# Kernel tuning notes

Measured on AMD Instinct MI355X. Metric: run time of the kernel, lower is better.

Reference implementation:

```python
import jax, jax.numpy as jnp
import numpy as np

V, D, DC, L, K, H, ND, S, B = 16, 256, 128, 3, 16, 4, 3, 900, 16
HD = D // H
DMETA = 17           # [confidence(1) | layer_id(8) | iter(4) | pass(4)]
DSLOT = DC + DMETA
MAX_ITERS, MAX_PASSES, WRITE_TOK = 2, 2, 64
FLOATS = ['token_embed','segment_embed','slot_embeddings','layer_id_embeddings',
          'Wq_read','Wk_read','Wv_read','Wg_read','bg_read','Wqkv','Wo',
          'Wwk','Wwv','Wwg','bwg','Wout','bout','prev_answer_embed','Wfb','bfb']


def setup_inputs():
    key = jax.random.key(0)
    ks = jax.random.split(key, 24)
    n = lambda i, shape: 0.02 * jax.random.normal(ks[i], shape, dtype=jnp.float32)
    return dict(
        demo_inputs=jax.random.randint(ks[0], (B, ND, S), 0, V),
        demo_outputs=jax.random.randint(ks[1], (B, ND, S), 0, V),
        test_input=jax.random.randint(ks[2], (B, S), 0, V),
        token_embed=n(3, (V, D)), segment_embed=n(4, (2, D)),
        slot_embeddings=n(5, (L, K, DC)), layer_id_embeddings=n(6, (L, 8)),
        Wq_read=n(7, (L, D, DC)), Wk_read=n(8, (L, DSLOT, DC)), Wv_read=n(9, (L, DSLOT, D)),
        Wg_read=n(10, (L, D, 1)), bg_read=jnp.zeros((L, 1)),
        Wqkv=n(11, (L, D, 3 * D)), Wo=n(12, (L, D, D)),
        Wwk=n(13, (L, D, DC)), Wwv=n(14, (L, D, DC)),
        Wwg=n(15, (L, 2 * DC, 1)), bwg=jnp.zeros((L, 1)),
        Wout=n(16, (D, V)), bout=jnp.zeros((V,)),
        prev_answer_embed=n(17, (V, D)),
        Wfb=n(18, (2 * D, D)), bfb=jnp.zeros((D,)),
    )


def make_rope(n, hd):
    inv = 1.0 / (10000.0 ** (jnp.arange(0, hd, 2, dtype=jnp.float32) / hd))
    f = jnp.arange(n, dtype=jnp.float32)[:, None] * inv[None, :]  # [N, hd/2]
    return jnp.cos(f), jnp.sin(f)


def apply_rope(x, cos, sin):  # x: [B,H,N,hd]
    x1, x2 = x[..., ::2], x[..., 1::2]
    r1 = x1 * cos - x2 * sin
    r2 = x1 * sin + x2 * cos
    return jnp.stack([r1, r2], axis=-1).reshape(x.shape)


def layer_step(h, cache, l, it, pas, cos, sin, p):
    Bsz, N, _ = h.shape
    s0 = l * K
    # --- read: cross-attention from sequence to full structured cache ---
    q = h @ p['Wq_read'][l]                                   # [B,N,DC]
    k = cache @ p['Wk_read'][l]                               # [B,LK,DC]
    v = cache @ p['Wv_read'][l]                               # [B,LK,D]
    attn = jax.nn.softmax(jnp.einsum('bnd,bmd->bnm', q, k) / np.float32(np.sqrt(DC)), axis=-1)
    read = jnp.einsum('bnm,bmd->bnd', attn, v)
    rgate = jax.nn.sigmoid(h @ p['Wg_read'][l] + p['bg_read'][l])
    h = h + rgate * read
    # --- linear self-attention with RoPE (use_linear_attention=True) ---
    qh, kh, vh = jnp.split(h @ p['Wqkv'][l], 3, axis=-1)
    heads = lambda x: x.reshape(Bsz, N, H, HD).transpose(0, 2, 1, 3)
    qh, kh, vh = heads(qh), heads(kh), heads(vh)
    qf = jax.nn.elu(apply_rope(qh, cos, sin)) + 1.0
    kf = jax.nn.elu(apply_rope(kh, cos, sin)) + 1.0
    kv = jnp.einsum('bhnd,bhne->bhde', kf, vh)                # [B,H,HD,HD]
    z = 1.0 / (jnp.einsum('bhnd,bhd->bhn', qf, kf.sum(axis=2)) + 1e-6)
    att = jnp.einsum('bhnd,bhde->bhne', qf, kv) * z[..., None]
    h = h + att.transpose(0, 2, 1, 3).reshape(Bsz, N, D) @ p['Wo'][l]
    # --- write: last max_write_tokens tokens -> this layer's slot block ---
    wt = h[:, -WRITE_TOK:]                                    # [B,64,D]
    wk, wv = wt @ p['Wwk'][l], wt @ p['Wwv'][l]               # [B,64,DC]
    sq = cache[:, s0:s0 + K, :DC]                             # slot content queries
    wattn = jax.nn.softmax(jnp.einsum('bkd,bmd->bkm', sq, wk) / np.float32(np.sqrt(DC)), axis=-1)
    new_c = jnp.einsum('bkm,bmd->bkd', wattn, wv)
    wgate = jax.nn.sigmoid(jnp.concatenate([sq, new_c], -1) @ p['Wwg'][l] + p['bwg'][l])
    it_oh = jax.nn.one_hot(min(it, 3), 4, dtype=h.dtype)
    ps_oh = jax.nn.one_hot(min(pas, 3), 4, dtype=h.dtype)
    cache = cache.at[:, s0:s0 + K, :DC].set(sq + wgate * new_c)
    cache = cache.at[:, s0:s0 + K, DC:DC + 1].set(wgate)      # confidence
    cache = cache.at[:, s0:s0 + K, DC + 9:DC + 13].set(jnp.broadcast_to(it_oh, (Bsz, K, 4)))
    cache = cache.at[:, s0:s0 + K, DC + 13:].set(jnp.broadcast_to(ps_oh, (Bsz, K, 4)))
    return h, cache


def _model(p, demo_inputs, demo_outputs, test_input):
    Bsz = test_input.shape[0]
    # interleave demo_in/demo_out pairs then append test input
    demos = jnp.stack([demo_inputs, demo_outputs], axis=2).reshape(Bsz, ND * 2 * S)
    full = jnp.concatenate([demos, test_input], axis=1)       # [B, 6300]
    N = full.shape[1]
    cur = p['token_embed'][full] + p['segment_embed'][0]      # [B,N,D]
    cos, sin = make_rope(N, HD)
    # initial cache: learned content | conf=0 | layer_id | iter=0 | pass=0
    content = jnp.broadcast_to(p['slot_embeddings'].reshape(L * K, DC), (Bsz, L * K, DC))
    lids = jnp.broadcast_to(p['layer_id_embeddings'][:, None, :], (L, K, 8)).reshape(L * K, 8)
    meta = jnp.concatenate([jnp.zeros((L * K, 1)), lids, jnp.zeros((L * K, 8))], axis=-1)
    cache = jnp.concatenate([content, jnp.broadcast_to(meta, (Bsz, L * K, DMETA))], axis=-1)
    ts = ND * 2 * S
    prev_logits = None
    for pas in range(MAX_PASSES):
        if pas > 0:  # answer feedback from previous pass predictions
            pae = p['prev_answer_embed'][jnp.argmax(prev_logits, axis=-1)]
            tr = cur[:, ts:ts + S]
            g = jax.nn.sigmoid(jnp.concatenate([tr, pae], -1) @ p['Wfb'] + p['bfb'])
            cur = cur.at[:, ts:ts + S].set(tr + g * pae)
        h = cur
        for l in range(L):
            for it in range(MAX_ITERS):
                h, cache = layer_step(h, cache, l, it, pas, cos, sin, p)
        prev_logits = h[:, ts:ts + S] @ p['Wout'] + p['bout']  # [B,S,V]
    return prev_logits


def reference(demo_inputs, demo_outputs, test_input, token_embed, segment_embed,
              slot_embeddings, layer_id_embeddings, Wq_read, Wk_read, Wv_read,
              Wg_read, bg_read, Wqkv, Wo, Wwk, Wwv, Wwg, bwg, Wout, bout,
              prev_answer_embed, Wfb, bfb):
    p = dict(zip(FLOATS, (token_embed, segment_embed, slot_embeddings, layer_id_embeddings,
                          Wq_read, Wk_read, Wv_read, Wg_read, bg_read, Wqkv, Wo,
                          Wwk, Wwv, Wwg, bwg, Wout, bout, prev_answer_embed, Wfb, bfb)))
    return _model(p, demo_inputs, demo_outputs, test_input)
```

## Files before the change

### kernel.cpp

```cpp
#include <hip/hip_runtime.h>
#include <math.h>

#define Bz 16
#define Sz 900
#define Vz 16
#define Dz 256
#define DCz 128
#define Hz 4
#define Nz 6300
#define TSz 5400
#define DSLOTz 145
#define NSLOTz 48
#define GXA 99

typedef unsigned short u16;
typedef unsigned int u32;

typedef __bf16 bf16x8 __attribute__((ext_vector_type(8)));
typedef float floatx4 __attribute__((ext_vector_type(4)));
union U8 { bf16x8 v; uint4 q; };

static __device__ __forceinline__ float sigm(float x){ return 1.0f/(1.0f+__expf(-x)); }
static __device__ __forceinline__ void fma4(float4& a, float s, float4 b){ a.x+=s*b.x; a.y+=s*b.y; a.z+=s*b.z; a.w+=s*b.w; }
static __device__ __forceinline__ float dot4(float4 a, float4 b){ return a.x*b.x + a.y*b.y + a.z*b.z + a.w*b.w; }
static __device__ __forceinline__ float4 f4z(){ float4 z; z.x=0.f; z.y=0.f; z.z=0.f; z.w=0.f; return z; }
static __device__ __forceinline__ float elu1(float x){ return x>0.f ? x+1.f : __expf(x); }
static __device__ __forceinline__ float fcomp(float4 v, int i){ return (i==0)?v.x:(i==1)?v.y:(i==2)?v.z:v.w; }

static __device__ __forceinline__ uint hi16(float x){
  uint u = __float_as_uint(x);
  return (u + 0x7fffu + ((u>>16)&1u)) >> 16;
}

typedef const void GV __attribute__((address_space(1)));
typedef void LV __attribute__((address_space(3)));
static __device__ __forceinline__ void gl16(const float* g, float* l){
  __builtin_amdgcn_global_load_lds((GV*)g, (LV*)l, 16, 0, 0);
}
static __device__ __forceinline__ void gl16b(const void* g, void* l){
  __builtin_amdgcn_global_load_lds((GV*)g, (LV*)l, 16, 0, 0);
}

__global__ void k_sentinel(float* out, int nelem){
  int i = blockIdx.x*256 + threadIdx.x;
  if (i < nelem) out[i] = 12345.0f;
}

__global__ void k_zero(float* p, int n){
  int i = blockIdx.x*256 + threadIdx.x;
  if (i < n) p[i] = 0.f;
}

__global__ void k_rope(float* cost, float* sint){
  int i = blockIdx.x*256 + threadIdx.x;
  if (i >= Nz*32) return;
  int n = i>>5, f = i&31;
  double invd = pow(10000.0, -(double)f/32.0);
  double fr = (double)n * invd;
  cost[i] = (float)cos(fr);
  sint[i] = (float)sin(fr);
}

__global__ void k_embed(const int* __restrict__ di, const int* __restrict__ dq,
                        const int* __restrict__ ti, const float* __restrict__ temb,
                        const float* __restrict__ semb, float* __restrict__ h){
  int i = blockIdx.x*256 + threadIdx.x;
  if (i >= Bz*Nz*64) return;
  int dv = i & 63; int bn = i >> 6; int n = bn % Nz; int b = bn / Nz;
  int tok;
  if (n < TSz){
    int nd = n/1800; int r = n - nd*1800;
    tok = (r < Sz) ? di[(b*3+nd)*Sz + r] : dq[(b*3+nd)*Sz + (r-Sz)];
  } else {
    tok = ti[b*Sz + (n-TSz)];
  }
  const float4* e4 = (const float4*)(temb + (size_t)tok*Dz);
  const float4* s4 = (const float4*)semb;
  float4 v = e4[dv]; float4 s = s4[dv];
  v.x += s.x; v.y += s.y; v.z += s.z; v.w += s.w;
  ((float4*)h)[(size_t)bn*64 + dv] = v;
}

__global__ void k_cache_init(const float* __restrict__ slot_emb, const float* __restrict__ lid,
                             float* __restrict__ cache){
  int i = blockIdx.x*256 + threadIdx.x;
  if (i >= Bz*NSLOTz*DSLOTz) return;
  int c = i % DSLOTz; int sc = (i / DSLOTz) % NSLOTz; int l = sc >> 4;
  float v = 0.f;
  if (c < DCz) v = slot_emb[sc*DCz + c];
  else if (c >= 129 && c < 137) v = lid[l*8 + (c-129)];
  cache[i] = v;
}

__global__ void k_pack_w(const float* __restrict__ Wqkv,
                         u16* __restrict__ wh, u16* __restrict__ wl){
  int i = blockIdx.x*256 + threadIdx.x;
  if (i >= 3*65536) return;
  int l = i >> 16; int r = i & 65535;
  int ks = r >> 13; int ct = (r>>9)&15; int lane = (r>>3)&63; int e = r&7;
  int k = ks*32 + ((lane>>4)<<3) + e;
  int c = ct*16 + (lane&15);
  float x = Wqkv[(size_t)l*196608 + (size_t)k*768 + c];
  uint hb = hi16(x);
  uint lb = hi16(x - __uint_as_float(hb<<16));
  wh[i] = (u16)hb; wl[i] = (u16)lb;
}

__global__ void k_pack_wkv(const float* __restrict__ Wqkv,
                           u16* __restrict__ wh, u16* __restrict__ wl){
  int i = blockIdx.x*256 + threadIdx.x;
  if (i >= 3*131072) return;
  int l = i / 131072; int r = i % 131072;
  int ks = r >> 14; int ct = (r>>9)&31; int lane = (r>>3)&63; int e = r&7;
  int k = ks*32 + ((lane>>4)<<3) + e;
  int c = ct*16 + (lane&15);
  float x = Wqkv[(size_t)l*196608 + (size_t)k*768 + 256 + c];
  uint hb = hi16(x);
  uint lb = hi16(x - __uint_as_float(hb<<16));
  wh[i] = (u16)hb; wl[i] = (u16)lb;
}

__global__ void k_pack_wr(const float* __restrict__ Wqr,
                          u16* __restrict__ wh, u16* __restrict__ wl){
  int i = blockIdx.x*256 + threadIdx.x;
  if (i >= 3*32768) return;
  int l = i >> 15; int r = i & 32767;
  int ks = r >> 12; int ct = (r>>9)&7; int lane = (r>>3)&63; int e = r&7;
  int k = ks*32 + ((lane>>4)<<3) + e;
  int c = ct*16 + (lane&15);
  float x = Wqr[(size_t)l*32768 + (size_t)k*DCz + c];
  uint hb = hi16(x);
  uint lb = hi16(x - __uint_as_float(hb<<16));
  wh[i] = (u16)hb; wl[i] = (u16)lb;
}

__global__ void k_pack_p(const float* __restrict__ pmat,
                         u16* __restrict__ ph, u16* __restrict__ pl){
  int i = blockIdx.x*256 + threadIdx.x;
  if (i >= 16*65536) return;
  int b = i >> 16; int r = i & 65535;
  int ks2 = r >> 13; int ct = (r>>9)&15; int lane = (r>>3)&63; int e = r&7;
  int c = ks2*32 + ((lane>>4)<<3) + e;
  int oc = ct*16 + (lane&15);
  float x = pmat[(((size_t)(b*4 + (c>>6)))*64 + (c&63))*256 + oc];
  uint hb = hi16(x);
  uint lb = hi16(x - __uint_as_float(hb<<16));
  ph[i] = (u16)hb; pl[i] = (u16)lb;
}

__global__ __launch_bounds__(384) void k_proj_cache(const float* __restrict__ cache,
    const float* __restrict__ Wk, const float* __restrict__ Wv,
    u16* __restrict__ krh, u16* __restrict__ krl,
    u16* __restrict__ vrh, u16* __restrict__ vrl){
  __shared__ float crow[DSLOTz];
  int b = blockIdx.x / NSLOTz, sc = blockIdx.x % NSLOTz;
  int t = threadIdx.x;
  const float* cp = cache + (size_t)(b*NSLOTz+sc)*DSLOTz;
  if (t < DSLOTz) crow[t] = cp[t];
  __syncthreads();
  if (t < DCz){
    float a = 0.f;
    for (int r2=0;r2<DSLOTz;r2++) a += crow[r2]*Wk[r2*DCz + t];
    uint hb = hi16(a);
    uint lb = hi16(a - __uint_as_float(hb<<16));
    int ks = t>>5, st = sc>>4, lane = (sc&15) | (((t>>3)&3)<<4), e = t&7;
    size_t idx = (size_t)b*6144 + (size_t)(((ks*3+st)*64 + lane)*8 + e);
    krh[idx] = (u16)hb; krl[idx] = (u16)lb;
  } else {
    int d = t - DCz;
    float a = 0.f;
    for (int r2=0;r2<DSLOTz;r2++) a += crow[r2]*Wv[r2*Dz + d];
    uint hb = hi16(a);
    uint lb = hi16(a - __uint_as_float(hb<<16));
    int ot = d>>4, ks2 = sc>>5, lane = (d&15) | (((sc>>3)&3)<<4), e = sc&7;
    size_t idx = (size_t)b*16384 + (size_t)(((ks2*16+ot)*64 + lane)*8 + e);
    vrh[idx] = (u16)hb; vrl[idx] = (u16)lb;
  }
}

#define RA2_BH 0
#define RA2_BL 5120
#define RA2_QBH 10240
#define RA2_QBL 30720
#define RA2_ABH 10240
#define RA2_ABL 20480
#define RA2_G  51200
#define RA2_WG 51456
__global__ __launch_bounds__(256) void k_read_attn(
    float* __restrict__ h,
    const u16* __restrict__ wqh, const u16* __restrict__ wql,
    const u16* __restrict__ krh, const u16* __restrict__ krl,
    const u16* __restrict__ vrh, const u16* __restrict__ vrl,
    const float* __restrict__ Wg, const float* __restrict__ bg){
  __shared__ float smem[13120];
  char* sb = (char*)smem;
  const int t = threadIdx.x;
  const int b = blockIdx.y;
  const int n0 = blockIdx.x*64;
  const int w = t>>6, lane = t&63, ln = t&15, lq = (t>>4)&3;
  float* hb = h + (size_t)b*Nz*Dz;
  ((float*)(sb+RA2_WG))[t] = Wg[t];
  floatx4 acc[2][4];
  #pragma unroll
  for (int i=0;i<2;i++)
    #pragma unroll
    for (int j=0;j<4;j++){ acc[i][j][0]=0.f; acc[i][j][1]=0.f; acc[i][j][2]=0.f; acc[i][j][3]=0.f; }
  for (int ks=0; ks<8; ks++){
    __syncthreads();
    {
      int n = n0 + (t>>2);
      const float* hp = hb + (size_t)n*Dz + ks*32 + (t&3)*8;
      float x[8];
      if (n < Nz){
        float4 v0 = *(const float4*)(hp);
        float4 v1 = *(const float4*)(hp+4);
        x[0]=v0.x; x[1]=v0.y; x[2]=v0.z; x[3]=v0.w;
        x[4]=v1.x; x[5]=v1.y; x[6]=v1.z; x[7]=v1.w;
      } else {
        #pragma unroll
        for (int e=0;e<8;e++) x[e]=0.f;
      }
      uint hw[4], lw[4];
      #pragma unroll
      for (int e=0;e<4;e++){
        uint h0=hi16(x[2*e]), h1=hi16(x[2*e+1]);
        uint l0=hi16(x[2*e]-__uint_as_float(h0<<16));
        uint l1=hi16(x[2*e+1]-__uint_as_float(h1<<16));
        hw[e]=h0|(h1<<16); lw[e]=l0|(l1<<16);
      }
      int a16 = (((t>>2)*5 + (t&3))<<4);
      *(uint4*)(sb + RA2_BH + a16) = make_uint4(hw[0],hw[1],hw[2],hw[3]);
      *(uint4*)(sb + RA2_BL + a16) = make_uint4(lw[0],lw[1],lw[2],lw[3]);
    }
    __syncthreads();
    U8 bh[4], bl[4];
    #pragma unroll
    for (int nt=0; nt<4; nt++){
      int a16 = (((nt*16+ln)*5 + lq)<<4);
      bh[nt].q = *(const uint4*)(sb + RA2_BH + a16);
      bl[nt].q = *(const uint4*)(sb + RA2_BL + a16);
    }
    #pragma unroll
    for (int mf=0; mf<2; mf++){
      U8 ah, al;
      size_t ai = ((size_t)(ks*8 + w*2 + mf))*512 + lane*8;
      ah.q = *(const uint4*)(wqh + ai);
      al.q = *(const uint4*)(wql + ai);
      #pragma unroll
      for (int nt=0; nt<4; nt++){
        acc[mf][nt] = __builtin_amdgcn_mfma_f32_16x16x32_bf16(ah.v, bh[nt].v, acc[mf][nt], 0,0,0);
        acc[mf][nt] = __builtin_amdgcn_mfma_f32_16x16x32_bf16(ah.v, bl[nt].v, acc[mf][nt], 0,0,0);
        acc[mf][nt] = __builtin_amdgcn_mfma_f32_16x16x32_bf16(al.v, bh[nt].v, acc[mf][nt], 0,0,0);
      }
    }
  }
  {
    int n = t>>2, kq = t&3;
    int nn = n0+n; int nc = (nn < Nz) ? nn : (Nz-1);
    const float* hp = hb + (size_t)nc*Dz + kq*64;
    const float* wgp = (const float*)(sb+RA2_WG) + kq*64;
    float a = 0.f;
    for (int k=0;k<64;k+=4){
      float4 hv = *(const float4*)(hp+k);
      float4 wv = *(const float4*)(wgp+k);
      a += dot4(hv,wv);
    }
    a += __shfl_xor(a,1,64);
    a += __shfl_xor(a,2,64);
    if (kq==0) ((float*)(sb+RA2_G))[n] = a;
  }
  {
    #pragma unroll
    for (int mf=0; mf<2; mf++){
      #pragma unroll
      for (int nt=0; nt<4; nt++){
        float v0 = acc[mf][nt][0], v1 = acc[mf][nt][1];
        float v2 = acc[mf][nt][2], v3 = acc[mf][nt][3];
        uint h0=hi16(v0), h1=hi16(v1), h2=hi16(v2), h3=hi16(v3);
        uint l0=hi16(v0-__uint_as_float(h0<<16));
        uint l1=hi16(v1-__uint_as_float(h1<<16));
        uint l2=hi16(v2-__uint_as_float(h2<<16));
        uint l3=hi16(v3-__uint_as_float(h3<<16));
        int a16 = (((nt*16+ln)*5 + (mf*2 + (lq>>1)))<<4) + ((lq&1)<<3);
        *(uint2*)(sb + RA2_QBH + w*5120 + a16) = make_uint2(h0|(h1<<16), h2|(h3<<16));
        *(uint2*)(sb + RA2_QBL + w*5120 + a16) = make_uint2(l0|(l1<<16), l2|(l3<<16));
      }
    }
  }
  __syncthreads();
  floatx4 sacc[3];
  #pragma unroll
  for (int st=0; st<3; st++){ sacc[st][0]=0.f; sacc[st][1]=0.f; sacc[st][2]=0.f; sacc[st][3]=0.f; }
  for (int ks=0; ks<4; ks++){
    U8 bh, bl;
    int a16 = (((w*16+ln)*5 + lq)<<4);
    bh.q = *(const uint4*)(sb + RA2_QBH + ks*5120 + a16);
    bl.q = *(const uint4*)(sb + RA2_QBL + ks*5120 + a16);
    #pragma unroll
    for (int st=0; st<3; st++){
      U8 ah, al;
      size_t ai = (size_t)b*6144 + ((size_t)(ks*3+st))*512 + lane*8;
      ah.q = *(const uint4*)(krh + ai);
      al.q = *(const uint4*)(krl + ai);
      sacc[st] = __builtin_amdgcn_mfma_f32_16x16x32_bf16(ah.v, bh.v, sacc[st], 0,0,0);
      sacc[st] = __builtin_amdgcn_mfma_f32_16x16x32_bf16(ah.v, bl.v, sacc[st], 0,0,0);
      sacc[st] = __builtin_amdgcn_mfma_f32_16x16x32_bf16(al.v, bh.v, sacc[st], 0,0,0);
    }
  }
  {
    const float scl = 0.088388347648318447f;
    float mx = -1e30f;
    #pragma unroll
    for (int st=0; st<3; st++)
      #pragma unroll
      for (int r=0;r<4;r++){ sacc[st][r] *= scl; mx = fmaxf(mx, sacc[st][r]); }
    mx = fmaxf(mx, __shfl_xor(mx, 16, 64));
    mx = fmaxf(mx, __shfl_xor(mx, 32, 64));
    float su = 0.f;
    #pragma unroll
    for (int st=0; st<3; st++)
      #pragma unroll
      for (int r=0;r<4;r++){ float e = __expf(sacc[st][r]-mx); sacc[st][r]=e; su+=e; }
    su += __shfl_xor(su, 16, 64);
    su += __shfl_xor(su, 32, 64);
    float inv = 1.f/su;
    #pragma unroll
    for (int st=0; st<3; st++)
      #pragma unroll
      for (int r=0;r<4;r++) sacc[st][r] *= inv;
  }
  __syncthreads();
  {
    uint2 ah2[3], al2[3];
    #pragma unroll
    for (int st=0; st<3; st++){
      float v0=sacc[st][0], v1=sacc[st][1], v2=sacc[st][2], v3=sacc[st][3];
      uint h0=hi16(v0), h1=hi16(v1), h2=hi16(v2), h3=hi16(v3);
      uint l0=hi16(v0-__uint_as_float(h0<<16));
      uint l1=hi16(v1-__uint_as_float(h1<<16));
      uint l2=hi16(v2-__uint_as_float(h2<<16));
      uint l3=hi16(v3-__uint_as_float(h3<<16));
      ah2[st] = make_uint2(h0|(h1<<16), h2|(h3<<16));
      al2[st] = make_uint2(l0|(l1<<16), l2|(l3<<16));
    }
    int rb = (w*16+ln)*5;
    int sub = (lq&1)<<3;
    #pragma unroll
    for (int st=0; st<2; st++){
      int a16 = ((rb + st*2 + (lq>>1))<<4) + sub;
      *(uint2*)(sb + RA2_ABH + a16) = ah2[st];
      *(uint2*)(sb + RA2_ABL + a16) = al2[st];
    }
    {
      int a16 = ((rb + (lq>>1))<<4) + sub;
      *(uint2*)(sb + RA2_ABH + 5120 + a16) = ah2[2];
      *(uint2*)(sb + RA2_ABL + 5120 + a16) = al2[2];
      int z16 = ((rb + 2 + (lq>>1))<<4) + sub;
      *(uint2*)(sb + RA2_ABH + 5120 + z16) = make_uint2(0,0);
      *(uint2*)(sb + RA2_ABL + 5120 + z16) = make_uint2(0,0);
    }
  }
  __syncthreads();
  floatx4 o[4][4];
  #pragma unroll
  for (int i=0;i<4;i++)
    #pragma unroll
    for (int j=0;j<4;j++){ o[i][j][0]=0.f; o[i][j][1]=0.f; o[i][j][2]=0.f; o[i][j][3]=0.f; }
  #pragma unroll
  for (int ks2=0; ks2<2; ks2++){
    U8 bh[4], bl[4];
    #pragma unroll
    for (int nt=0; nt<4; nt++){
      int a16 = (((nt*16+ln)*5 + lq)<<4);
      bh[nt].q = *(const uint4*)(sb + RA2_ABH + ks2*5120 + a16);
      bl[nt].q = *(const uint4*)(sb + RA2_ABL + ks2*5120 + a16);
    }
    #pragma unroll
    for (int mf=0; mf<4; mf++){
      U8 ah, al;
      size_t ai = (size_t)b*16384 + ((size_t)(ks2*16 + w*4 + mf))*512 + lane*8;
      ah.q = *(const uint4*)(vrh + ai);
      al.q = *(const uint4*)(vrl + ai);
      #pragma unroll
      for (int nt=0; nt<4; nt++){
        o[mf][nt] = __builtin_amdgcn_mfma_f32_16x16x32_bf16(ah.v, bh[nt].v, o[mf][nt], 0,0,0);
        o[mf][nt] = __builtin_amdgcn_mfma_f32_16x16x32_bf16(ah.v, bl[nt].v, o[mf][nt], 0,0,0);
        o[mf][nt] = __builtin_amdgcn_mfma_f32_16x16x32_bf16(al.v, bh[nt].v, o[mf][nt], 0,0,0);
      }
    }
  }
  float bg0 = bg[0];
  #pragma unroll
  for (int nt=0; nt<4; nt++){
    int n = n0 + nt*16 + ln;
    if (n < Nz){
      float gv = sigm(((const float*)(sb+RA2_G))[nt*16+ln] + bg0);
      #pragma unroll
      for (int mf=0; mf<4; mf++){
        float* hp = hb + (size_t)n*Dz + w*64 + mf*16 + lq*4;
        float4 hv = *(const float4*)hp;
        hv.x += gv*o[mf][nt][0];
        hv.y += gv*o[mf][nt][1];
        hv.z += gv*o[mf][nt][2];
        hv.w += gv*o[mf][nt][3];
        *(float4*)hp = hv;
      }
    }
  }
}

#define KV_BH 0
#define KV_BL 5120
__global__ __launch_bounds__(256) void k_kv(
    const float* __restrict__ h,
    const u16* __restrict__ wh, const u16* __restrict__ wl,
    const float* __restrict__ cost, const float* __restrict__ sint,
    float* __restrict__ kvpart, float* __restrict__ kvbuf, int use_part){
  __shared__ float smem[8704];
  char* sb = (char*)smem;
  const int t = threadIdx.x;
  const int b = blockIdx.y;
  const int n0 = blockIdx.x*64;
  const int w = t>>6;
  const int lane = t&63;
  const int ln = t&15;
  const int lq = (t>>4)&3;
  const float* hb = h + (size_t)b*Nz*Dz;
  floatx4 acc[2][4][4];
  #pragma unroll
  for (int cp=0;cp<2;cp++)
    #pragma unroll
    for (int i=0;i<4;i++)
      #pragma unroll
      for (int j=0;j<4;j++){ acc[cp][i][j][0]=0.f; acc[cp][i][j][1]=0.f; acc[cp][i][j][2]=0.f; acc[cp][i][j][3]=0.f; }

  for (int ks=0; ks<8; ks++){
    __syncthreads();
    {
      int n = n0 + (t>>2);
      const float* hp = hb + (size_t)n*Dz + ks*32 + (t&3)*8;
      float x[8];
      if (n < Nz){
        float4 v0 = *(const float4*)(hp);
        float4 v1 = *(const float4*)(hp+4);
        x[0]=v0.x; x[1]=v0.y; x[2]=v0.z; x[3]=v0.w;
        x[4]=v1.x; x[5]=v1.y; x[6]=v1.z; x[7]=v1.w;
      } else {
        #pragma unroll
        for (int e=0;e<8;e++) x[e]=0.f;
      }
      uint hw[4], lw[4];
      #pragma unroll
      for (int e=0;e<4;e++){
        uint h0=hi16(x[2*e]), h1=hi16(x[2*e+1]);
        uint l0=hi16(x[2*e]-__uint_as_float(h0<<16));
        uint l1=hi16(x[2*e+1]-__uint_as_float(h1<<16));
        hw[e]=h0|(h1<<16); lw[e]=l0|(l1<<16);
      }
      int a16 = (((t>>2)*5 + (t&3))<<4);
      *(uint4*)(sb + KV_BH + a16) = make_uint4(hw[0],hw[1],hw[2],hw[3]);
      *(uint4*)(sb + KV_BL + a16) = make_uint4(lw[0],lw[1],lw[2],lw[3]);
    }
    __syncthreads();
    U8 bh[4], bl[4];
    #pragma unroll
    for (int nt=0; nt<4; nt++){
      int a16 = (((nt*16+ln)*5 + lq)<<4);
      bh[nt].q = *(const uint4*)(sb + KV_BH + a16);
      bl[nt].q = *(const uint4*)(sb + KV_BL + a16);
    }
    #pragma unroll
    for (int cp=0; cp<2; cp++){
      #pragma unroll
      for (int mf=0; mf<4; mf++){
        U8 ah, al;
        size_t ai = ((size_t)(ks*32 + cp*16 + w*4 + mf))*512 + lane*8;
        ah.q = *(const uint4*)(wh + ai);
        al.q = *(const uint4*)(wl + ai);
        #pragma unroll
        for (int nt=0; nt<4; nt++){
          acc[cp][mf][nt] = __builtin_amdgcn_mfma_f32_16x16x32_bf16(ah.v, bh[nt].v, acc[cp][mf][nt], 0,0,0);
          acc[cp][mf][nt] = __builtin_amdgcn_mfma_f32_16x16x32_bf16(ah.v, bl[nt].v, acc[cp][mf][nt], 0,0,0);
          acc[cp][mf][nt] = __builtin_amdgcn_mfma_f32_16x16x32_bf16(al.v, bh[nt].v, acc[cp][mf][nt], 0,0,0);
        }
      }
    }
  }
  #pragma unroll
  for (int mf=0; mf<4; mf++){
    #pragma unroll
    for (int nt=0; nt<4; nt++){
      int n = n0 + nt*16 + ln;
      int valid = (n < Nz);
      int nc = valid ? n : (Nz-1);
      int pi = mf*8 + lq*2;
      float2 c2 = *(const float2*)(cost + (size_t)nc*32 + pi);
      float2 s2 = *(const float2*)(sint + (size_t)nc*32 + pi);
      float q0 = acc[0][mf][nt][0], q1 = acc[0][mf][nt][1];
      float q2 = acc[0][mf][nt][2], q3 = acc[0][mf][nt][3];
      float r0 = elu1(q0*c2.x - q1*s2.x);
      float r1 = elu1(q0*s2.x + q1*c2.x);
      float r2 = elu1(q2*c2.y - q3*s2.y);
      float r3 = elu1(q2*s2.y + q3*c2.y);
      acc[0][mf][nt][0] = valid ? r0 : 0.f;
      acc[0][mf][nt][1] = valid ? r1 : 0.f;
      acc[0][mf][nt][2] = valid ? r2 : 0.f;
      acc[0][mf][nt][3] = valid ? r3 : 0.f;
    }
  }
  const int d = t&63, q4 = t>>6;
  float* kfL = smem;
  float* vL  = smem + 4352;
  for (int g=0; g<4; g++){
    __syncthreads();
    if (w == g){
      #pragma unroll
      for (int mf=0; mf<4; mf++){
        #pragma unroll
        for (int nt=0; nt<4; nt++){
          int n = nt*16 + ln;
          int cc = mf*16 + lq*4;
          *(float4*)(kfL + n*68 + cc) = make_float4(acc[0][mf][nt][0],acc[0][mf][nt][1],acc[0][mf][nt][2],acc[0][mf][nt][3]);
          *(float4*)(vL  + n*68 + cc) = make_float4(acc[1][mf][nt][0],acc[1][mf][nt][1],acc[1][mf][nt][2],acc[1][mf][nt][3]);
        }
      }
    }
    __syncthreads();
    float4 kvacc[4];
    #pragma unroll
    for (int u=0;u<4;u++) kvacc[u]=f4z();
    float ksl = 0.f;
    for (int row=0; row<64; row++){
      float kd = kfL[row*68 + d];
      ksl += kd;
      const float4* vp = (const float4*)(vL + row*68);
      #pragma unroll
      for (int u=0;u<4;u++) fma4(kvacc[u], kd, vp[q4*4+u]);
    }
    if (use_part){
      float* kq = kvpart + ((size_t)((b*Hz + g)*GXA) + blockIdx.x)*4160;
      #pragma unroll
      for (int u=0;u<4;u++){
        int e = q4*16 + 4*u;
        kq[(e+0)*64+d] = kvacc[u].x;
        kq[(e+1)*64+d] = kvacc[u].y;
        kq[(e+2)*64+d] = kvacc[u].z;
        kq[(e+3)*64+d] = kvacc[u].w;
      }
      if (q4==0) kq[4096+d] = ksl;
    } else {
      float* kq = kvbuf + ((size_t)(b*Hz + g))*4160;
      #pragma unroll
      for (int u=0;u<4;u++){
        int e = q4*16 + 4*u;
        atomicAdd(&kq[(e+0)*64+d], kvacc[u].x);
        atomicAdd(&kq[(e+1)*64+d], kvacc[u].y);
        atomicAdd(&kq[(e+2)*64+d], kvacc[u].z);
        atomicAdd(&kq[(e+3)*64+d], kvacc[u].w);
      }
      if (q4==0) atomicAdd(&kq[4096+d], ksl);
    }
  }
}

__global__ __launch_bounds__(256) void k_pmat(
    const float* __restrict__ kvpart, float* __restrict__ kvbuf,
    const float* __restrict__ Wo, float* __restrict__ pmat, int use_part){
  __shared__ float smem[8448];
  const int t = threadIdx.x;
  const int bh = blockIdx.x;
  const int hh = bh & 3;
  const int c0 = t&15, rr = t>>4;
  if (use_part){
    const float* pp = kvpart + (size_t)bh*GXA*4160;
    for (int id=t; id<4160; id+=256){
      float a = 0.f;
      for (int bx=0; bx<GXA; bx++) a += pp[(size_t)bx*4160 + id];
      if (id < 4096) smem[(id>>6)*68 + (id&63)] = a;
      else kvbuf[(size_t)bh*4160 + id] = a;
    }
  } else {
    const float* kvp = kvbuf + (size_t)bh*4160;
    for (int id=t; id<4096; id+=256){
      int e=id>>6, d=id&63;
      smem[e*68+d] = kvp[id];
    }
  }
  float4 acc[4][4];
  #pragma unroll
  for (int i=0;i<4;i++){
    #pragma unroll
    for (int j=0;j<4;j++) acc[i][j]=f4z();
  }
  for (int kt=0; kt<64; kt+=16){
    __syncthreads();
    for (int id=t; id<1024; id+=256){
      int wr=id>>6, cf=id&63;
      ((float4*)(smem+4352))[wr*64+cf] = ((const float4*)(Wo + (size_t)(hh*64+kt+wr)*256))[cf];
    }
    __syncthreads();
    for (int kk=0; kk<16; kk++){
      float4 a4 = *(const float4*)(smem + (kt+kk)*68 + 4*rr);
      const float4* wrow = (const float4*)(smem+4352) + kk*64;
      float4 w0=wrow[c0], w1=wrow[c0+16], w2=wrow[c0+32], w3=wrow[c0+48];
      #pragma unroll
      for (int i=0;i<4;i++){
        float ac = fcomp(a4,i);
        fma4(acc[i][0],ac,w0); fma4(acc[i][1],ac,w1); fma4(acc[i][2],ac,w2); fma4(acc[i][3],ac,w3);
      }
    }
  }
  float* Pp = pmat + (size_t)bh*16384;
  #pragma unroll
  for (int i=0;i<4;i++){
    #pragma unroll
    for (int j=0;j<4;j++) ((float4*)Pp)[(4*rr+i)*64 + c0 + 16*j] = acc[i][j];
  }
}

#define AH_OFF 0
#define AL_OFF 16384
#define BH_OFF 32768
#define BL_OFF 37888
#define KS_OFF 43008
__global__ __launch_bounds__(256) void k_att(
    float* __restrict__ h,
    const u16* __restrict__ wqh, const u16* __restrict__ wql,
    const u16* __restrict__ pth, const u16* __restrict__ ptl,
    const float* __restrict__ kvbuf,
    const float* __restrict__ cost, const float* __restrict__ sint){
  __shared__ float smem[11008];
  char* sb = (char*)smem;
  const int t = threadIdx.x;
  const int b = blockIdx.y;
  const int n0 = blockIdx.x*64;
  const int w = t>>6;
  const int lane = t&63;
  const int ln = t&15;
  const int lq = (t>>4)&3;
  float* hb = h + (size_t)b*Nz*Dz;
  ((float*)(sb+KS_OFF))[t] = kvbuf[(size_t)(b*Hz + w)*4160 + 4096 + lane];
  floatx4 acc[4][4];
  #pragma unroll
  for (int i=0;i<4;i++)
    #pragma unroll
    for (int j=0;j<4;j++){ acc[i][j][0]=0.f; acc[i][j][1]=0.f; acc[i][j][2]=0.f; acc[i][j][3]=0.f; }

  for (int ks=0; ks<8; ks++){
    __syncthreads();
    const u16* sh = wqh + (size_t)ks*8192;
    const u16* sl = wql + (size_t)ks*8192;
    #pragma unroll
    for (int j=0;j<4;j++){
      int c = w*4 + j;
      gl16b(sh + c*512 + lane*8, sb + AH_OFF + c*1024);
      gl16b(sl + c*512 + lane*8, sb + AL_OFF + c*1024);
    }
    {
      int n = n0 + (t>>2);
      const float* hp = hb + (size_t)n*Dz + ks*32 + (t&3)*8;
      float x[8];
      if (n < Nz){
        float4 v0 = *(const float4*)(hp);
        float4 v1 = *(const float4*)(hp+4);
        x[0]=v0.x; x[1]=v0.y; x[2]=v0.z; x[3]=v0.w;
        x[4]=v1.x; x[5]=v1.y; x[6]=v1.z; x[7]=v1.w;
      } else {
        #pragma unroll
        for (int e=0;e<8;e++) x[e]=0.f;
      }
      uint hw[4], lw[4];
      #pragma unroll
      for (int e=0;e<4;e++){
        uint h0=hi16(x[2*e]), h1=hi16(x[2*e+1]);
        uint l0=hi16(x[2*e]-__uint_as_float(h0<<16));
        uint l1=hi16(x[2*e+1]-__uint_as_float(h1<<16));
        hw[e]=h0|(h1<<16); lw[e]=l0|(l1<<16);
      }
      int a16 = (((t>>2)*5 + (t&3))<<4);
      *(uint4*)(sb + BH_OFF + a16) = make_uint4(hw[0],hw[1],hw[2],hw[3]);
      *(uint4*)(sb + BL_OFF + a16) = make_uint4(lw[0],lw[1],lw[2],lw[3]);
    }
    __syncthreads();
    U8 bh[4], bl[4];
    #pragma unroll
    for (int nt=0; nt<4; nt++){
      int a16 = (((nt*16+ln)*5 + lq)<<4);
      bh[nt].q = *(const uint4*)(sb + BH_OFF + a16);
      bl[nt].q = *(const uint4*)(sb + BL_OFF + a16);
    }
    #pragma unroll
    for (int mf=0; mf<4; mf++){
      U8 ah, al;
      int a16 = (((w*4+mf)*64 + lane)<<4);
      ah.q = *(const uint4*)(sb + AH_OFF + a16);
      al.q = *(const uint4*)(sb + AL_OFF + a16);
      #pragma unroll
      for (int nt=0; nt<4; nt++){
        acc[mf][nt] = __builtin_amdgcn_mfma_f32_16x16x32_bf16(ah.v, bh[nt].v, acc[mf][nt], 0,0,0);
        acc[mf][nt] = __builtin_amdgcn_mfma_f32_16x16x32_bf16(ah.v, bl[nt].v, acc[mf][nt], 0,0,0);
        acc[mf][nt] = __builtin_amdgcn_mfma_f32_16x16x32_bf16(al.v, bh[nt].v, acc[mf][nt], 0,0,0);
      }
    }
  }
  uint2 qzh[4][4], qzl[4][4];
  {
    float4 ks4[4];
    #pragma unroll
    for (int mf=0; mf<4; mf++)
      ks4[mf] = *(const float4*)(sb + KS_OFF + ((w*64 + mf*16 + lq*4)<<2));
    float psum[4] = {0.f,0.f,0.f,0.f};
    #pragma unroll
    for (int mf=0; mf<4; mf++){
      #pragma unroll
      for (int nt=0; nt<4; nt++){
        int n = n0 + nt*16 + ln;
        int nc = (n < Nz) ? n : (Nz-1);
        int pi = mf*8 + lq*2;
        float2 c2 = *(const float2*)(cost + (size_t)nc*32 + pi);
        float2 s2 = *(const float2*)(sint + (size_t)nc*32 + pi);
        float q0 = acc[mf][nt][0], q1 = acc[mf][nt][1];
        float q2 = acc[mf][nt][2], q3 = acc[mf][nt][3];
        float r0 = elu1(q0*c2.x - q1*s2.x);
        float r1 = elu1(q0*s2.x + q1*c2.x);
        float r2 = elu1(q2*c2.y - q3*s2.y);
        float r3 = elu1(q2*s2.y + q3*c2.y);
        acc[mf][nt][0]=r0; acc[mf][nt][1]=r1; acc[mf][nt][2]=r2; acc[mf][nt][3]=r3;
        psum[nt] += r0*ks4[mf].x + r1*ks4[mf].y + r2*ks4[mf].z + r3*ks4[mf].w;
      }
    }
    float zt[4];
    #pragma unroll
    for (int nt=0; nt<4; nt++){
      float p = psum[nt];
      p += __shfl_xor(p, 16, 64);
      p += __shfl_xor(p, 32, 64);
      zt[nt] = 1.f/(p + 1e-6f);
    }
    #pragma unroll
    for (int mf=0; mf<4; mf++){
      #pragma unroll
      for (int nt=0; nt<4; nt++){
        float v0 = acc[mf][nt][0]*zt[nt];
        float v1 = acc[mf][nt][1]*zt[nt];
        float v2 = acc[mf][nt][2]*zt[nt];
        float v3 = acc[mf][nt][3]*zt[nt];
        uint h0=hi16(v0), h1=hi16(v1), h2=hi16(v2), h3=hi16(v3);
        qzh[mf][nt] = make_uint2(h0|(h1<<16), h2|(h3<<16));
        uint l0=hi16(v0-__uint_as_float(h0<<16));
        uint l1=hi16(v1-__uint_as_float(h1<<16));
        uint l2=hi16(v2-__uint_as_float(h2<<16));
        uint l3=hi16(v3-__uint_as_float(h3<<16));
        qzl[mf][nt] = make_uint2(l0|(l1<<16), l2|(l3<<16));
      }
    }
  }
  floatx4 acc2[4][4];
  #pragma unroll
  for (int i=0;i<4;i++)
    #pragma unroll
    for (int j=0;j<4;j++){ acc2[i][j][0]=0.f; acc2[i][j][1]=0.f; acc2[i][j][2]=0.f; acc2[i][j][3]=0.f; }
  for (int ks2=0; ks2<8; ks2++){
    __syncthreads();
    const u16* sh = pth + (size_t)(b*8 + ks2)*8192;
    const u16* sl = ptl + (size_t)(b*8 + ks2)*8192;
    #pragma unroll
    for (int j=0;j<4;j++){
      int c = w*4 + j;
      gl16b(sh + c*512 + lane*8, sb + AH_OFF + c*1024);
// ... 93 lines not shown
    int k2 = t>>4;
    const float4* s4 = (const float4*)(sqL) + k2*33;
    for (int mm=0;mm<4;mm++){
      int m = (t&15) + 16*mm;
      const float4* k4 = (const float4*)(wkL) + m*33;
      float a=0.f;
      for (int d4=0;d4<32;d4++) a += dot4(s4[d4], k4[d4]);
      wat[k2*68+m] = a * 0.088388347648318447f;
    }
  }
  __syncthreads();
  if (t<16){
    float mx=-1e30f;
    for (int m=0;m<64;m++) mx = fmaxf(mx, wat[t*68+m]);
    float su=0.f;
    for (int m=0;m<64;m++){ float e=__expf(wat[t*68+m]-mx); wat[t*68+m]=e; su+=e; }
    float inv=1.f/su;
    for (int m=0;m<64;m++) wat[t*68+m]*=inv;
  }
  __syncthreads();
  {
    int k2=t>>4, c0=t&15;
    float4 a0=f4z(), a1=f4z();
    const float4* wvg = (const float4*)(wvbuf + (size_t)b*64*DCz);
    for (int m=0;m<64;m++){
      float a = wat[k2*68+m];
      fma4(a0,a,wvg[m*32+c0]); fma4(a1,a,wvg[m*32+c0+16]);
    }
    ((float4*)ncL)[k2*33+c0]=a0; ((float4*)ncL)[k2*33+16+c0]=a1;
  }
  __syncthreads();
  if (t<16){
    float a = bwg[0];
    for (int d2=0; d2<DCz; d2++) a += sqL[t*132+d2]*Wwg[d2] + ncL[t*132+d2]*Wwg[DCz+d2];
    wg[t] = sigm(a);
  }
  __syncthreads();
  for (int i=t;i<16*DCz;i+=256){
    int k2=i>>7,c=i&127;
    cache[((size_t)(b*NSLOTz)+s0+k2)*DSLOTz + c] = sqL[k2*132+c] + wg[k2]*ncL[k2*132+c];
  }
  if (t<16){
    float* cp = cache + ((size_t)(b*NSLOTz)+s0+t)*DSLOTz;
    cp[128] = wg[t];
    cp[137] = (it==0)?1.f:0.f; cp[138] = (it==1)?1.f:0.f; cp[139]=0.f; cp[140]=0.f;
    cp[141] = (pas==0)?1.f:0.f; cp[142] = (pas==1)?1.f:0.f; cp[143]=0.f; cp[144]=0.f;
  }
}

__global__ __launch_bounds__(256) void k_logits(const float* __restrict__ h,
    const float* __restrict__ Wout, const float* __restrict__ bout, float* __restrict__ out){
  __shared__ float hl[16*257];
  int t = threadIdx.x; int row0 = blockIdx.x*16;
  for (int i=t;i<16*Dz;i+=256){
    int rr=i>>8,c=i&255; int row=row0+rr; int b=row/Sz, s=row-b*Sz;
    hl[rr*257+c] = h[((size_t)b*Nz + TSz + s)*Dz + c];
  }
  __syncthreads();
  int rr = t>>4, v = t&15;
  float a = bout[v];
  for (int c=0;c<Dz;c++) a += hl[rr*257+c]*Wout[c*Vz + v];
  out[(size_t)(row0+rr)*Vz + v] = a;
}

__global__ __launch_bounds__(256) void k_feedback(float* __restrict__ h,
    const float* __restrict__ logits0, const float* __restrict__ pae,
    const float* __restrict__ Wfb, const float* __restrict__ bfb){
  __shared__ float trL[16*257];
  __shared__ float paeL[16*257];
  __shared__ int amL[16];
  int t = threadIdx.x; int b = blockIdx.y; int s0 = blockIdx.x*16;
  if (t<16){
    int s = s0+t; int am=0;
    if (s < Sz){
      const float* lg = logits0 + (size_t)(b*Sz+s)*Vz;
      float best = lg[0];
      for (int v=1;v<16;v++){ if (lg[v] > best){ best=lg[v]; am=v; } }
    }
    amL[t]=am;
  }
  for (int i=t;i<16*Dz;i+=256){
    int rr=i>>8,c=i&255; int s=s0+rr;
    trL[rr*257+c] = (s<Sz)? h[((size_t)b*Nz + TSz + s)*Dz + c] : 0.f;
  }
  __syncthreads();
  for (int i=t;i<16*Dz;i+=256){ int rr=i>>8,c=i&255; paeL[rr*257+c] = pae[(size_t)amL[rr]*Dz + c]; }
  __syncthreads();
  int r=t>>4, c0=t&15;
  float4 acc[4]; acc[0]=f4z(); acc[1]=f4z(); acc[2]=f4z(); acc[3]=f4z();
  for (int kk=0;kk<Dz;kk++){
    float xv = trL[r*257+kk];
    const float4* wr = (const float4*)(Wfb + (size_t)kk*Dz);
    fma4(acc[0],xv,wr[c0]); fma4(acc[1],xv,wr[c0+16]); fma4(acc[2],xv,wr[c0+32]); fma4(acc[3],xv,wr[c0+48]);
  }
  for (int kk=0;kk<Dz;kk++){
    float xv = paeL[r*257+kk];
    const float4* wr = (const float4*)(Wfb + (size_t)(Dz+kk)*Dz);
    fma4(acc[0],xv,wr[c0]); fma4(acc[1],xv,wr[c0+16]); fma4(acc[2],xv,wr[c0+32]); fma4(acc[3],xv,wr[c0+48]);
  }
  int s = s0+r;
  if (s < Sz){
    float* cp = h + ((size_t)b*Nz + TSz + s)*Dz;
    #pragma unroll
    for (int j=0;j<4;j++){
      float vals[4] = {acc[j].x, acc[j].y, acc[j].z, acc[j].w};
      #pragma unroll
      for (int q2=0;q2<4;q2++){
        int c = (c0+16*j)*4 + q2;
        float g = sigm(vals[q2] + bfb[c]);
        cp[c] = trL[r*257+c] + g*paeL[r*257+c];
      }
    }
  }
}

extern "C" void kernel_launch(void* const* d_in, const int* in_sizes, int n_in,
                              void* d_out, int out_size, void* d_ws, size_t ws_size,
                              hipStream_t stream){
  (void)in_sizes; (void)n_in;
  const int*   demo_in   = (const int*)d_in[0];
  const int*   demo_out  = (const int*)d_in[1];
  const int*   test_in   = (const int*)d_in[2];
  const float* token_emb = (const float*)d_in[3];
  const float* seg_emb   = (const float*)d_in[4];
  const float* slot_emb  = (const float*)d_in[5];
  const float* lid_emb   = (const float*)d_in[6];
  const float* Wq_read   = (const float*)d_in[7];
  const float* Wk_read   = (const float*)d_in[8];
  const float* Wv_read   = (const float*)d_in[9];
  const float* Wg_read   = (const float*)d_in[10];
  const float* bg_read   = (const float*)d_in[11];
  const float* Wqkv      = (const float*)d_in[12];
  const float* Wo        = (const float*)d_in[13];
  const float* Wwk       = (const float*)d_in[14];
  const float* Wwv       = (const float*)d_in[15];
  const float* Wwg       = (const float*)d_in[16];
  const float* bwg       = (const float*)d_in[17];
  const float* Wout      = (const float*)d_in[18];
  const float* bout      = (const float*)d_in[19];
  const float* pae       = (const float*)d_in[20];
  const float* Wfb       = (const float*)d_in[21];
  const float* bfb       = (const float*)d_in[22];

  char* wsb = (char*)d_ws;
  size_t off = 0;
  auto alloc = [&](size_t bytes)->char*{
    char* p = wsb + off;
    off += (bytes + 255) & ~(size_t)255;
    return p;
  };
  float* hbuf   = (float*)alloc((size_t)Bz*Nz*Dz*4);
  float* cache  = (float*)alloc((size_t)Bz*NSLOTz*DSLOTz*4);
  float* kvbuf  = (float*)alloc((size_t)Bz*Hz*4160*4);
  float* pmat   = (float*)alloc((size_t)Bz*Hz*64*256*4);
  float* wkbuf  = (float*)alloc((size_t)Bz*64*DCz*4);
  float* wvbuf  = (float*)alloc((size_t)Bz*64*DCz*4);
  float* logits0= (float*)alloc((size_t)Bz*Sz*Vz*4);
  float* cost   = (float*)alloc((size_t)Nz*32*4);
  float* sint   = (float*)alloc((size_t)Nz*32*4);
  u16*   wqth   = (u16*)alloc((size_t)3*65536*2);
  u16*   wqtl   = (u16*)alloc((size_t)3*65536*2);
  u16*   pth    = (u16*)alloc((size_t)16*65536*2);
  u16*   ptl    = (u16*)alloc((size_t)16*65536*2);
  u16*   wkvh   = (u16*)alloc((size_t)3*131072*2);
  u16*   wkvl   = (u16*)alloc((size_t)3*131072*2);
  u16*   wqrh   = (u16*)alloc((size_t)3*32768*2);
  u16*   wqrl   = (u16*)alloc((size_t)3*32768*2);
  u16*   krh    = (u16*)alloc((size_t)Bz*6144*2);
  u16*   krl    = (u16*)alloc((size_t)Bz*6144*2);
  u16*   vrh    = (u16*)alloc((size_t)Bz*16384*2);
  u16*   vrl    = (u16*)alloc((size_t)Bz*16384*2);

  size_t off_base = off;
  if (off_base > ws_size){
    k_sentinel<<<(out_size+255)/256, 256, 0, stream>>>((float*)d_out, out_size);
    return;
  }
  float* kvpart = (float*)alloc((size_t)Bz*Hz*GXA*4160*4);
  int use_part = (off <= ws_size) ? 1 : 0;
  if (!use_part){ off = off_base; kvpart = kvbuf;  }

  k_rope<<<(Nz*32+255)/256, 256, 0, stream>>>(cost, sint);
  k_cache_init<<<(Bz*NSLOTz*DSLOTz+255)/256, 256, 0, stream>>>(slot_emb, lid_emb, cache);
  k_pack_w<<<768, 256, 0, stream>>>(Wqkv, wqth, wqtl);
  k_pack_wkv<<<1536, 256, 0, stream>>>(Wqkv, wkvh, wkvl);
  k_pack_wr<<<384, 256, 0, stream>>>(Wq_read, wqrh, wqrl);
  k_zero<<<512, 256, 0, stream>>>((float*)vrh, Bz*16384/2);
  k_zero<<<512, 256, 0, stream>>>((float*)vrl, Bz*16384/2);

  const int KVN = Bz*Hz*4160;
  for (int pas=0; pas<2; pas++){
    k_embed<<<(Bz*Nz*64+255)/256, 256, 0, stream>>>(demo_in, demo_out, test_in, token_emb, seg_emb, hbuf);
    if (pas==1)
      k_feedback<<<dim3(57,Bz), 256, 0, stream>>>(hbuf, logits0, pae, Wfb, bfb);
    for (int l=0; l<3; l++){
      for (int it=0; it<2; it++){
        k_proj_cache<<<Bz*NSLOTz, 384, 0, stream>>>(cache,
            Wk_read + (size_t)l*DSLOTz*DCz, Wv_read + (size_t)l*DSLOTz*Dz,
            krh, krl, vrh, vrl);
        k_read_attn<<<dim3(GXA,Bz), 256, 0, stream>>>(hbuf,
            wqrh + (size_t)l*32768, wqrl + (size_t)l*32768,
            krh, krl, vrh, vrl,
            Wg_read + (size_t)l*Dz, bg_read + l);
        if (!use_part)
          k_zero<<<(KVN+255)/256, 256, 0, stream>>>(kvbuf, KVN);
        k_kv<<<dim3(GXA,Bz), 256, 0, stream>>>(hbuf,
            wkvh + (size_t)l*131072, wkvl + (size_t)l*131072, cost, sint,
            kvpart, kvbuf, use_part);
        k_pmat<<<Bz*Hz, 256, 0, stream>>>(kvpart, kvbuf, Wo + (size_t)l*Dz*Dz, pmat, use_part);
        k_pack_p<<<4096, 256, 0, stream>>>(pmat, pth, ptl);
        k_att<<<dim3(GXA,Bz), 256, 0, stream>>>(hbuf,
            wqth + (size_t)l*65536, wqtl + (size_t)l*65536, pth, ptl,
            kvbuf, cost, sint);
        k_wkv<<<dim3(4,Bz), 256, 0, stream>>>(hbuf,
            Wwk + (size_t)l*Dz*DCz, Wwv + (size_t)l*Dz*DCz, wkbuf, wvbuf);
        k_cache_upd<<<Bz, 256, 0, stream>>>(cache, wkbuf, wvbuf,
            Wwg + (size_t)l*2*DCz, bwg + l, l*16, it, pas);
      }
    }
    float* outp = (pas==0) ? logits0 : (float*)d_out;
    k_logits<<<900, 256, 0, stream>>>(hbuf, Wout, bout, outp);
  }
}
```

Before: 9.425 ms.

## Double-buffer h tiles in k_kv, use atomic KV reduction, fuse P packing into k_pmat

k_kv now prefetches the next h slice into registers while running MFMAs on the current one, and alternates between two shared-memory buffers so one barrier per k-step is enough. The per-block partial KV buffer and its serial 99-way reduction in k_pmat are replaced by atomicAdd into a zeroed kvbuf. k_pmat now writes the bf16 hi/lo packed P layout directly, which removes the separate k_pack_p launch and the fp32 pmat round trip. In exchange, atomics add contention and make summation order nondeterministic, and the fused pack uses scattered 2-byte stores.

```diff
diff --git a/kernel.cpp b/kernel.cpp
--- a/kernel.cpp
+++ b/kernel.cpp
@@ -132,20 +132,6 @@
   uint hb = hi16(x);
   uint lb = hi16(x - __uint_as_float(hb<<16));
   wh[i] = (u16)hb; wl[i] = (u16)lb;
-}
-
-__global__ void k_pack_p(const float* __restrict__ pmat,
-                         u16* __restrict__ ph, u16* __restrict__ pl){
-  int i = blockIdx.x*256 + threadIdx.x;
-  if (i >= 16*65536) return;
-  int b = i >> 16; int r = i & 65535;
-  int ks2 = r >> 13; int ct = (r>>9)&15; int lane = (r>>3)&63; int e = r&7;
-  int c = ks2*32 + ((lane>>4)<<3) + e;
-  int oc = ct*16 + (lane&15);
-  float x = pmat[(((size_t)(b*4 + (c>>6)))*64 + (c&63))*256 + oc];
-  uint hb = hi16(x);
-  uint lb = hi16(x - __uint_as_float(hb<<16));
-  ph[i] = (u16)hb; pl[i] = (u16)lb;
 }
 
 __global__ __launch_bounds__(384) void k_proj_cache(const float* __restrict__ cache,
@@ -409,13 +395,11 @@
   }
 }
 
-#define KV_BH 0
-#define KV_BL 5120
 __global__ __launch_bounds__(256) void k_kv(
     const float* __restrict__ h,
     const u16* __restrict__ wh, const u16* __restrict__ wl,
     const float* __restrict__ cost, const float* __restrict__ sint,
-    float* __restrict__ kvpart, float* __restrict__ kvbuf, int use_part){
+    float* __restrict__ kvbuf){
   __shared__ float smem[8704];
   char* sb = (char*)smem;
   const int t = threadIdx.x;
@@ -434,40 +418,47 @@
       #pragma unroll
       for (int j=0;j<4;j++){ acc[cp][i][j][0]=0.f; acc[cp][i][j][1]=0.f; acc[cp][i][j][2]=0.f; acc[cp][i][j][3]=0.f; }
 
+  const int hrow = t>>2, hcol = t&3;
+  const float* hbase = hb + (size_t)(n0+hrow)*Dz + hcol*8;
+  const int hvalid = (n0+hrow) < Nz;
+  const int a16w = ((hrow*5 + hcol)<<4);
+
+  auto load_h = [&](int ks, float x[8]){
+    if (hvalid){
+      float4 v0 = *(const float4*)(hbase + ks*32);
+      float4 v1 = *(const float4*)(hbase + ks*32 + 4);
+      x[0]=v0.x; x[1]=v0.y; x[2]=v0.z; x[3]=v0.w;
+      x[4]=v1.x; x[5]=v1.y; x[6]=v1.z; x[7]=v1.w;
+    } else {
+      #pragma unroll
+      for (int e=0;e<8;e++) x[e]=0.f;
+    }
+  };
+  auto cvt_write = [&](const float x[8], int buf){
+    uint hw[4], lw[4];
+    #pragma unroll
+    for (int e=0;e<4;e++){
+      uint h0=hi16(x[2*e]), h1=hi16(x[2*e+1]);
+      uint l0=hi16(x[2*e]-__uint_as_float(h0<<16));
+      uint l1=hi16(x[2*e+1]-__uint_as_float(h1<<16));
+      hw[e]=h0|(h1<<16); lw[e]=l0|(l1<<16);
+    }
+    *(uint4*)(sb + buf*10240 + a16w) = make_uint4(hw[0],hw[1],hw[2],hw[3]);
+    *(uint4*)(sb + buf*10240 + 5120 + a16w) = make_uint4(lw[0],lw[1],lw[2],lw[3]);
+  };
+
+  { float x0[8]; load_h(0, x0); cvt_write(x0, 0); }
   for (int ks=0; ks<8; ks++){
     __syncthreads();
-    {
-      int n = n0 + (t>>2);
-      const float* hp = hb + (size_t)n*Dz + ks*32 + (t&3)*8;
-      float x[8];
-      if (n < Nz){
-        float4 v0 = *(const float4*)(hp);
-        float4 v1 = *(const float4*)(hp+4);
-        x[0]=v0.x; x[1]=v0.y; x[2]=v0.z; x[3]=v0.w;
-        x[4]=v1.x; x[5]=v1.y; x[6]=v1.z; x[7]=v1.w;
-      } else {
-        #pragma unroll
-        for (int e=0;e<8;e++) x[e]=0.f;
-      }
-      uint hw[4], lw[4];
-      #pragma unroll
-      for (int e=0;e<4;e++){
-        uint h0=hi16(x[2*e]), h1=hi16(x[2*e+1]);
-        uint l0=hi16(x[2*e]-__uint_as_float(h0<<16));
-        uint l1=hi16(x[2*e+1]-__uint_as_float(h1<<16));
-        hw[e]=h0|(h1<<16); lw[e]=l0|(l1<<16);
-      }
-      int a16 = (((t>>2)*5 + (t&3))<<4);
-      *(uint4*)(sb + KV_BH + a16) = make_uint4(hw[0],hw[1],hw[2],hw[3]);
-      *(uint4*)(sb + KV_BL + a16) = make_uint4(lw[0],lw[1],lw[2],lw[3]);
-    }
-    __syncthreads();
+    float xn[8];
+    if (ks < 7) load_h(ks+1, xn);
+    const int cb = ks&1;
     U8 bh[4], bl[4];
     #pragma unroll
     for (int nt=0; nt<4; nt++){
       int a16 = (((nt*16+ln)*5 + lq)<<4);
-      bh[nt].q = *(const uint4*)(sb + KV_BH + a16);
-      bl[nt].q = *(const uint4*)(sb + KV_BL + a16);
+      bh[nt].q = *(const uint4*)(sb + cb*10240 + a16);
+      bl[nt].q = *(const uint4*)(sb + cb*10240 + 5120 + a16);
     }
     #pragma unroll
     for (int cp=0; cp<2; cp++){
@@ -485,6 +476,7 @@
         }
       }
     }
+    if (ks < 7) cvt_write(xn, cb^1);
   }
   #pragma unroll
   for (int mf=0; mf<4; mf++){
@@ -537,54 +529,32 @@
       #pragma unroll
       for (int u=0;u<4;u++) fma4(kvacc[u], kd, vp[q4*4+u]);
     }
-    if (use_part){
-      float* kq = kvpart + ((size_t)((b*Hz + g)*GXA) + blockIdx.x)*4160;
-      #pragma unroll
-      for (int u=0;u<4;u++){
-        int e = q4*16 + 4*u;
-        kq[(e+0)*64+d] = kvacc[u].x;
-        kq[(e+1)*64+d] = kvacc[u].y;
-        kq[(e+2)*64+d] = kvacc[u].z;
-        kq[(e+3)*64+d] = kvacc[u].w;
-      }
-      if (q4==0) kq[4096+d] = ksl;
-    } else {
-      float* kq = kvbuf + ((size_t)(b*Hz + g))*4160;
-      #pragma unroll
-      for (int u=0;u<4;u++){
-        int e = q4*16 + 4*u;
-        atomicAdd(&kq[(e+0)*64+d], kvacc[u].x);
-        atomicAdd(&kq[(e+1)*64+d], kvacc[u].y);
-        atomicAdd(&kq[(e+2)*64+d], kvacc[u].z);
-        atomicAdd(&kq[(e+3)*64+d], kvacc[u].w);
-      }
-      if (q4==0) atomicAdd(&kq[4096+d], ksl);
-    }
+    float* kq = kvbuf + ((size_t)(b*Hz + g))*4160;
+    #pragma unroll
+    for (int u=0;u<4;u++){
+      int e = q4*16 + 4*u;
+      atomicAdd(&kq[(e+0)*64+d], kvacc[u].x);
+      atomicAdd(&kq[(e+1)*64+d], kvacc[u].y);
+      atomicAdd(&kq[(e+2)*64+d], kvacc[u].z);
+      atomicAdd(&kq[(e+3)*64+d], kvacc[u].w);
+    }
+    if (q4==0) atomicAdd(&kq[4096+d], ksl);
   }
 }
 
 __global__ __launch_bounds__(256) void k_pmat(
-    const float* __restrict__ kvpart, float* __restrict__ kvbuf,
-    const float* __restrict__ Wo, float* __restrict__ pmat, int use_part){
+    const float* __restrict__ kvbuf, const float* __restrict__ Wo,
+    u16* __restrict__ ph, u16* __restrict__ pl){
   __shared__ float smem[8448];
   const int t = threadIdx.x;
   const int bh = blockIdx.x;
   const int hh = bh & 3;
+  const int bb = bh >> 2;
   const int c0 = t&15, rr = t>>4;
-  if (use_part){
-    const float* pp = kvpart + (size_t)bh*GXA*4160;
-    for (int id=t; id<4160; id+=256){
-      float a = 0.f;
-      for (int bx=0; bx<GXA; bx++) a += pp[(size_t)bx*4160 + id];
-      if (id < 4096) smem[(id>>6)*68 + (id&63)] = a;
-      else kvbuf[(size_t)bh*4160 + id] = a;
-    }
-  } else {
-    const float* kvp = kvbuf + (size_t)bh*4160;
-    for (int id=t; id<4096; id+=256){
-      int e=id>>6, d=id&63;
-      smem[e*68+d] = kvp[id];
-    }
+  const float* kvp = kvbuf + (size_t)bh*4160;
+  for (int id=t; id<4096; id+=256){
+    int e=id>>6, d=id&63;
+    smem[e*68+d] = kvp[id];
   }
   float4 acc[4][4];
   #pragma unroll
@@ -610,11 +580,26 @@
       }
     }
   }
-  float* Pp = pmat + (size_t)bh*16384;
   #pragma unroll
   for (int i=0;i<4;i++){
-    #pragma unroll
-    for (int j=0;j<4;j++) ((float4*)Pp)[(4*rr+i)*64 + c0 + 16*j] = acc[i][j];
+    int hd = 4*rr + i;
+    int e = hd & 7;
+    int ln4 = (hd>>3) & 3;
+    int ks2 = (hh*64 + hd) >> 5;
+    #pragma unroll
+    for (int j=0;j<4;j++){
+      float4 v = acc[i][j];
+      #pragma unroll
+      for (int q2=0;q2<4;q2++){
+        int oc = 4*c0 + 64*j + q2;
+        int ct = oc>>4, l15 = oc&15;
+        size_t idx = (size_t)bb*65536 + (((size_t)((ks2*16+ct)*64) + (l15 | (ln4<<4)))*8) + e;
+        float val = fcomp(v, q2);
+        uint hbt = hi16(val);
+        uint lbt = hi16(val - __uint_as_float(hbt<<16));
+        ph[idx] = (u16)hbt; pl[idx] = (u16)lbt;
+      }
+    }
   }
 }
 
@@ -1014,7 +999,6 @@
   float* hbuf   = (float*)alloc((size_t)Bz*Nz*Dz*4);
   float* cache  = (float*)alloc((size_t)Bz*NSLOTz*DSLOTz*4);
   float* kvbuf  = (float*)alloc((size_t)Bz*Hz*4160*4);
-  float* pmat   = (float*)alloc((size_t)Bz*Hz*64*256*4);
   float* wkbuf  = (float*)alloc((size_t)Bz*64*DCz*4);
   float* wvbuf  = (float*)alloc((size_t)Bz*64*DCz*4);
   float* logits0= (float*)alloc((size_t)Bz*Sz*Vz*4);
@@ -1033,14 +1017,10 @@
   u16*   vrh    = (u16*)alloc((size_t)Bz*16384*2);
   u16*   vrl    = (u16*)alloc((size_t)Bz*16384*2);
 
-  size_t off_base = off;
-  if (off_base > ws_size){
+  if (off > ws_size){
     k_sentinel<<<(out_size+255)/256, 256, 0, stream>>>((float*)d_out, out_size);
     return;
   }
-  float* kvpart = (float*)alloc((size_t)Bz*Hz*GXA*4160*4);
-  int use_part = (off <= ws_size) ? 1 : 0;
-  if (!use_part){ off = off_base; kvpart = kvbuf;  }
 
   k_rope<<<(Nz*32+255)/256, 256, 0, stream>>>(cost, sint);
   k_cache_init<<<(Bz*NSLOTz*DSLOTz+255)/256, 256, 0, stream>>>(slot_emb, lid_emb, cache);
@@ -1064,13 +1044,10 @@
             wqrh + (size_t)l*32768, wqrl + (size_t)l*32768,
             krh, krl, vrh, vrl,
             Wg_read + (size_t)l*Dz, bg_read + l);
-        if (!use_part)
-          k_zero<<<(KVN+255)/256, 256, 0, stream>>>(kvbuf, KVN);
+        k_zero<<<(KVN+255)/256, 256, 0, stream>>>(kvbuf, KVN);
         k_kv<<<dim3(GXA,Bz), 256, 0, stream>>>(hbuf,
-            wkvh + (size_t)l*131072, wkvl + (size_t)l*131072, cost, sint,
-            kvpart, kvbuf, use_part);
-        k_pmat<<<Bz*Hz, 256, 0, stream>>>(kvpart, kvbuf, Wo + (size_t)l*Dz*Dz, pmat, use_part);
-        k_pack_p<<<4096, 256, 0, stream>>>(pmat, pth, ptl);
+            wkvh + (size_t)l*131072, wkvl + (size_t)l*131072, cost, sint, kvbuf);
+        k_pmat<<<Bz*Hz, 256, 0, stream>>>(kvbuf, Wo + (size_t)l*Dz*Dz, pth, ptl);
         k_att<<<dim3(GXA,Bz), 256, 0, stream>>>(hbuf,
             wqth + (size_t)l*65536, wqtl + (size_t)l*65536, pth, ptl,
             kvbuf, cost, sint);
```

Result: faster. 8.334 ms (-11.6%).
